# Performance work log

Hardware: AMD Instinct MI355X
Metric: run time of the kernel (lower is better)

## Reference

```python
import jax, jax.numpy as jnp
import numpy as np

B, L1, L2, H = 32, 512, 512, 768


def setup_inputs() -> dict:
    key = jax.random.key(0)
    k1, k2, k3, k4 = jax.random.split(key, 4)
    x = jax.random.normal(k1, (B, L1, H), dtype=jnp.float32)
    y = jax.random.normal(k2, (B, L2, H), dtype=jnp.float32)
    # y_mask: True = padding position to be masked out (torch masked_fill semantics)
    y_mask = jax.random.randint(k3, (B, L2), 0, 2).astype(bool)
    W = jax.random.normal(k4, (H, H), dtype=jnp.float32) * 0.02  # nn.Linear weight [out,in]
    b = jnp.zeros((H,), dtype=jnp.float32)
    return {"x": x, "y": y, "y_mask": y_mask, "W": W, "b": b}


def reference(x, y, y_mask, W, b):
    # Shared linear projection + ReLU on both sequences (nn.Linear: v @ W^T + b)
    x_proj = jax.nn.relu(jnp.einsum('bmh,oh->bmo', x, W) + b)
    y_proj = jax.nn.relu(jnp.einsum('bnh,oh->bno', y, W) + b)
    # Unscaled attention scores [B, L1, L2]
    scores = jnp.einsum('bmh,bnh->bmn', x_proj, y_proj)
    scores = jnp.where(y_mask[:, None, :], -jnp.inf, scores)
    alpha = jax.nn.softmax(scores, axis=-1)
    # Attention-weighted sum over the *original* y (not y_proj)
    matched_seq = jnp.einsum('bmn,bnh->bmh', alpha, y)
    return matched_seq
```

## Files before the change

kernel.cpp:

```cpp
#include <hip/hip_runtime.h>
#include <hip/hip_bf16.h>
#include <math.h>


typedef _Float16 f16x8 __attribute__((ext_vector_type(8)));
typedef float f32x4 __attribute__((ext_vector_type(4)));

__device__ __forceinline__ void gld_lds16(const void* g, void* l) {
  __builtin_amdgcn_global_load_lds(
      (const __attribute__((address_space(1))) unsigned*)g,
      (__attribute__((address_space(3))) unsigned*)l, 16, 0, 0);
}

#define BARR()                          \
  do {                                  \
    __builtin_amdgcn_s_barrier();       \
    __builtin_amdgcn_sched_barrier(0);  \
  } while (0)
#define LGKM0()                                        \
  do {                                                 \
    asm volatile("s_waitcnt lgkmcnt(0)" ::: "memory"); \
    __builtin_amdgcn_sched_barrier(0);                 \
  } while (0)
#define VMW(n)                                            \
  do {                                                    \
    asm volatile("s_waitcnt vmcnt(" #n ")" ::: "memory"); \
    __builtin_amdgcn_sched_barrier(0);                    \
  } while (0)

__global__ __launch_bounds__(256) void cvt_xy_kernel(
    const float* __restrict__ x, const float* __restrict__ y,
    _Float16* __restrict__ xh, _Float16* __restrict__ yh) {
  const float* src = blockIdx.y ? y : x;
  _Float16* dst = blockIdx.y ? yh : xh;
  size_t i = ((size_t)blockIdx.x * 256 + threadIdx.x) * 8;
  float4 a = *(const float4*)&src[i];
  float4 b = *(const float4*)&src[i + 4];
  _Float16 h[8] = {(_Float16)a.x, (_Float16)a.y, (_Float16)a.z, (_Float16)a.w,
                   (_Float16)b.x, (_Float16)b.y, (_Float16)b.z, (_Float16)b.w};
  *(uint4*)&dst[i] = *(uint4*)h;
}

__global__ __launch_bounds__(256) void cvt_f16_kernel(
    const float* __restrict__ src, _Float16* __restrict__ dst) {
  size_t i = ((size_t)blockIdx.x * 256 + threadIdx.x) * 8;
  float4 a = *(const float4*)&src[i];
  float4 b = *(const float4*)&src[i + 4];
  _Float16 h[8] = {(_Float16)a.x, (_Float16)a.y, (_Float16)a.z, (_Float16)a.w,
                   (_Float16)b.x, (_Float16)b.y, (_Float16)b.z, (_Float16)b.w};
  *(uint4*)&dst[i] = *(uint4*)h;
}


__device__ __forceinline__ void stage128(const _Float16* __restrict__ G,
                                         int grow0, int k0, _Float16* L,
                                         int w, int l) {
#pragma unroll
  for (int s = 0; s < 2; ++s) {
    int rb = s * 64 + w * 8;
    int rin = rb + (l >> 3);
    int cp = (l & 7) ^ ((rin >> 1) & 6);
    gld_lds16(&G[(size_t)(grow0 + rin) * 768 + k0 + cp * 8],
              L + (size_t)rb * 64);
  }
}

__device__ __forceinline__ f16x8 frag_ld(const _Float16* S, int row, int colb) {
  int off = row * 128 + colb;
  off ^= (off >> 4) & 0x60;
  return *(const f16x8*)((const char*)S + off);
}

__device__ __forceinline__ void read_a(const _Float16* S, int wm, int mh,
                                       int fr, int fkg, f16x8 a[4][2]) {
#pragma unroll
  for (int f4 = 0; f4 < 4; ++f4)
#pragma unroll
    for (int ks = 0; ks < 2; ++ks)
      a[f4][ks] = frag_ld(S, wm + mh * 64 + f4 * 16 + fr, ks * 64 + fkg * 16);
}

__device__ __forceinline__ void read_b(const _Float16* S, int wn, int nf,
                                       int fr, int fkg, f16x8 b2[2]) {
#pragma unroll
  for (int ks = 0; ks < 2; ++ks)
    b2[ks] = frag_ld(S, wn + nf * 16 + fr, ks * 64 + fkg * 16);
}

__device__ __forceinline__ void mma8(f16x8 a[4][2], f16x8 b2[2],
                                     f32x4 acc[8][2], int mh, int nf) {
#pragma unroll
  for (int ks = 0; ks < 2; ++ks)
#pragma unroll
    for (int f4 = 0; f4 < 4; ++f4)
      acc[mh * 4 + f4][nf] = __builtin_amdgcn_mfma_f32_16x16x32_f16(
          a[f4][ks], b2[ks], acc[mh * 4 + f4][nf], 0, 0, 0);
}

__global__ __launch_bounds__(512, 2) void proj8_kernel(
    const _Float16* __restrict__ Xh, const _Float16* __restrict__ Yh,
    const _Float16* __restrict__ W, const float* __restrict__ bias,
    _Float16* __restrict__ Px, _Float16* __restrict__ Py) {
  const int N = 768;
  const _Float16* A = blockIdx.z ? Yh : Xh;
  _Float16* P = blockIdx.z ? Py : Px;
  extern __shared__ _Float16 smem[];
  _Float16* As0 = smem;
  _Float16* As1 = smem + 16384;
  _Float16* Bs0 = smem + 32768;
  _Float16* Bs1 = smem + 40960;

  const int bm = blockIdx.x * 256, bn = blockIdx.y * 128;
  const int tid = threadIdx.x, l = tid & 63, w = tid >> 6;
  const int fr = l & 15, fkg = l >> 4;
  const int wm = (w >> 2) * 128, wn = (w & 3) * 32;

  f32x4 acc[8][2];
#pragma unroll
  for (int i = 0; i < 8; ++i)
#pragma unroll
    for (int j = 0; j < 2; ++j)
#pragma unroll
      for (int e = 0; e < 4; ++e) acc[i][j][e] = 0.f;

  stage128(A, bm + 0, 0, As0, w, l);
  stage128(A, bm + 128, 0, As0 + 8192, w, l);
  stage128(W, bn, 0, Bs0, w, l);
  stage128(W, bn, 64, Bs1, w, l);
  VMW(2);
  BARR();

  f16x8 a[4][2], b0[2], b1[2];

  for (int t = 0; t < 6; ++t) {
    const bool g = (t < 5);
    const int ko = (2 * t + 1) * 64, ke = (2 * t + 2) * 64, kb = (2 * t + 3) * 64;
    read_a(As0, wm, 0, fr, fkg, a);
    read_b(Bs0, wn, 0, fr, fkg, b0);
    stage128(A, bm + 0, ko, As1, w, l);
    BARR(); LGKM0();
    __builtin_amdgcn_s_setprio(1);
    mma8(a, b0, acc, 0, 0);
    __builtin_amdgcn_s_setprio(0);
    BARR();
    read_b(Bs0, wn, 1, fr, fkg, b1);
    stage128(A, bm + 128, ko, As1 + 8192, w, l);
    BARR(); LGKM0();
    __builtin_amdgcn_s_setprio(1);
    mma8(a, b1, acc, 0, 1);
    __builtin_amdgcn_s_setprio(0);
    BARR();
    read_a(As0, wm, 1, fr, fkg, a);
    if (g) stage128(W, bn, ke, Bs0, w, l);
    BARR(); LGKM0();
    __builtin_amdgcn_s_setprio(1);
    mma8(a, b1, acc, 1, 1);
    mma8(a, b0, acc, 1, 0);
    __builtin_amdgcn_s_setprio(0);
    if (g) { VMW(2); } else { VMW(0); }
    BARR();
    read_a(As1, wm, 0, fr, fkg, a);
    read_b(Bs1, wn, 0, fr, fkg, b0);
    if (g) stage128(A, bm + 0, ke, As0, w, l);
    BARR(); LGKM0();
    __builtin_amdgcn_s_setprio(1);
    mma8(a, b0, acc, 0, 0);
    __builtin_amdgcn_s_setprio(0);
    BARR();
    read_b(Bs1, wn, 1, fr, fkg, b1);
    if (g) stage128(A, bm + 128, ke, As0 + 8192, w, l);
    BARR(); LGKM0();
    __builtin_amdgcn_s_setprio(1);
    mma8(a, b1, acc, 0, 1);
    __builtin_amdgcn_s_setprio(0);
    BARR();
    read_a(As1, wm, 1, fr, fkg, a);
    if (g) stage128(W, bn, kb, Bs1, w, l);
    BARR(); LGKM0();
    __builtin_amdgcn_s_setprio(1);
    mma8(a, b1, acc, 1, 1);
    mma8(a, b0, acc, 1, 0);
    __builtin_amdgcn_s_setprio(0);
    if (g) { VMW(2); } else { VMW(0); }
    BARR();
  }

#pragma unroll
  for (int mf = 0; mf < 8; ++mf)
#pragma unroll
    for (int r = 0; r < 4; ++r) {
      int m = bm + wm + mf * 16 + fkg * 4 + r;
#pragma unroll
      for (int nf = 0; nf < 2; ++nf) {
        int n = bn + wn + nf * 16 + fr;
        P[(size_t)m * N + n] = (_Float16)fmaxf(acc[mf][nf][r] + bias[n], 0.f);
      }
    }
}

__global__ __launch_bounds__(512) void scores_softmax_kernel(
    const _Float16* __restrict__ Px, const _Float16* __restrict__ Py,
    const int* __restrict__ mask, _Float16* __restrict__ Alpha) {
  const int K = 768, L = 512;
  __shared__ _Float16 As[64 * 32];
  __shared__ _Float16 Bs[512 * 32];
  __shared__ float redm[8][64], reds[8][64];
  int b = blockIdx.y;
  size_t pb = (size_t)b * L * K;
  const int* mk = mask + (size_t)b * L;
  _Float16* Ab = Alpha + (size_t)b * L * L;
  int bm = blockIdx.x * 64;
  int tid = threadIdx.x, lane = tid & 63, wave = tid >> 6;
  int wn = wave * 64;
  int fr = lane & 15, fk = (lane >> 4) * 8;
  int lrow = lane >> 2, lcol = (lane & 3) << 3;

  f32x4 acc[4][4];
#pragma unroll
  for (int i = 0; i < 4; ++i)
#pragma unroll
    for (int j = 0; j < 4; ++j)
#pragma unroll
      for (int e = 0; e < 4; ++e) acc[i][j][e] = 0.f;

  for (int k0 = 0; k0 < K; k0 += 32) {
    __syncthreads();
#pragma unroll
    for (int t = 0; t < 4; ++t) {
      int row = wave * 64 + t * 16;
      gld_lds16(&Py[pb + (size_t)(row + lrow) * K + k0 + lcol], &Bs[row * 32]);
    }
    if (wave < 4) {
      int row = wave * 16;
      gld_lds16(&Px[pb + (size_t)(bm + row + lrow) * K + k0 + lcol], &As[row * 32]);
    }
    __syncthreads();
    f16x8 a[4], bb[4];
#pragma unroll
    for (int i = 0; i < 4; ++i) {
      a[i] = *(const f16x8*)&As[(i * 16 + fr) * 32 + fk];
      bb[i] = *(const f16x8*)&Bs[(wn + i * 16 + fr) * 32 + fk];
    }
#pragma unroll
    for (int i = 0; i < 4; ++i)
#pragma unroll
      for (int j = 0; j < 4; ++j)
        acc[i][j] = __builtin_amdgcn_mfma_f32_16x16x32_f16(a[i], bb[j], acc[i][j], 0, 0, 0);
  }

  int mki[4];
#pragma unroll
  for (int j = 0; j < 4; ++j) mki[j] = mk[wn + j * 16 + fr];
#pragma unroll
  for (int i = 0; i < 4; ++i)
#pragma unroll
    for (int j = 0; j < 4; ++j)
      if (mki[j]) {
#pragma unroll
        for (int r = 0; r < 4; ++r) acc[i][j][r] = -INFINITY;
      }

  int g4 = (lane >> 4) << 2;
#pragma unroll
  for (int i = 0; i < 4; ++i)
#pragma unroll
    for (int r = 0; r < 4; ++r) {
      float m = fmaxf(fmaxf(acc[i][0][r], acc[i][1][r]),
                      fmaxf(acc[i][2][r], acc[i][3][r]));
      m = fmaxf(m, __shfl_xor(m, 1));
      m = fmaxf(m, __shfl_xor(m, 2));
      m = fmaxf(m, __shfl_xor(m, 4));
      m = fmaxf(m, __shfl_xor(m, 8));
      if (fr == 0) redm[wave][i * 16 + g4 + r] = m;
    }
  __syncthreads();
  float M[4][4];
#pragma unroll
  for (int i = 0; i < 4; ++i)
#pragma unroll
    for (int r = 0; r < 4; ++r) {
      int row = i * 16 + g4 + r;
      float m = redm[0][row];
#pragma unroll
      for (int ww = 1; ww < 8; ++ww) m = fmaxf(m, redm[ww][row]);
      M[i][r] = m;
    }
#pragma unroll
  for (int i = 0; i < 4; ++i)
#pragma unroll
    for (int r = 0; r < 4; ++r) {
      float s = 0.f;
#pragma unroll
      for (int j = 0; j < 4; ++j) {
        float e = __expf(acc[i][j][r] - M[i][r]);
        acc[i][j][r] = e;
        s += e;
      }
      s += __shfl_xor(s, 1);
      s += __shfl_xor(s, 2);
      s += __shfl_xor(s, 4);
      s += __shfl_xor(s, 8);
      if (fr == 0) reds[wave][i * 16 + g4 + r] = s;
    }
  __syncthreads();
#pragma unroll
  for (int i = 0; i < 4; ++i)
#pragma unroll
    for (int r = 0; r < 4; ++r) {
      int row = i * 16 + g4 + r;
      float s = reds[0][row];
#pragma unroll
      for (int ww = 1; ww < 8; ++ww) s += reds[ww][row];
      float inv = 1.0f / s;
#pragma unroll
      for (int j = 0; j < 4; ++j)
        Ab[(size_t)(bm + row) * L + wn + j * 16 + fr] =
            (_Float16)(acc[i][j][r] * inv);
    }
}

__global__ __launch_bounds__(256) void yT_kernel(
    const _Float16* __restrict__ Yh, _Float16* __restrict__ YT) {
  __shared__ unsigned short T[64][65];
  int b = blockIdx.z;
  int n0 = blockIdx.x * 64, h0 = blockIdx.y * 64;
  const unsigned short* Yb = (const unsigned short*)Yh + (size_t)b * 512 * 768;
  unsigned short* Tb = (unsigned short*)YT + (size_t)b * 768 * 512;
  int tid = threadIdx.x;
  int r = tid >> 4, c = (tid & 15) << 2;
#pragma unroll
  for (int i = 0; i < 4; ++i) {
    int rr = r + i * 16;
    ushort4 v = *(const ushort4*)&Yb[(size_t)(n0 + rr) * 768 + h0 + c];
    T[c + 0][rr] = v.x;
    T[c + 1][rr] = v.y;
    T[c + 2][rr] = v.z;
    T[c + 3][rr] = v.w;
  }
  __syncthreads();
  int hr = tid >> 2, nc = (tid & 3) << 4;
  unsigned short tmp[16];
#pragma unroll
  for (int j = 0; j < 16; ++j) tmp[j] = T[hr][nc + j];
  unsigned short* dst = &Tb[(size_t)(h0 + hr) * 512 + n0 + nc];
  *(uint4*)&dst[0] = *(uint4*)&tmp[0];
  *(uint4*)&dst[8] = *(uint4*)&tmp[8];
}

__global__ __launch_bounds__(256) void attn_mfma_kernel(
    const _Float16* __restrict__ Alpha, const _Float16* __restrict__ YT,
    float* __restrict__ O) {
  const int L = 512, H = 768;
  __shared__ _Float16 As[128 * 32], Bs[128 * 32];
  int b = blockIdx.z;
  const _Float16* Ab = Alpha + (size_t)b * L * L;
  const _Float16* Yb = YT + (size_t)b * H * L;
  float* Ob = O + (size_t)b * L * H;
  int bm = blockIdx.x * 128, bn = blockIdx.y * 128;
  int tid = threadIdx.x, lane = tid & 63, wave = tid >> 6;
  int wm = (wave & 1) * 64, wn = (wave >> 1) * 64;
  int fr = lane & 15, fk = (lane >> 4) * 8;
  int lrow = lane >> 2, lcol = (lane & 3) << 3;

  f32x4 acc[4][4];
#pragma unroll
  for (int i = 0; i < 4; ++i)
#pragma unroll
    for (int j = 0; j < 4; ++j)
#pragma unroll
      for (int e = 0; e < 4; ++e) acc[i][j][e] = 0.f;

  for (int k0 = 0; k0 < L; k0 += 32) {
    __syncthreads();
#pragma unroll
    for (int t = 0; t < 2; ++t) {
      int row = wave * 32 + t * 16;
      gld_lds16(&Ab[(size_t)(bm + row + lrow) * L + k0 + lcol], &As[row * 32]);
      gld_lds16(&Yb[(size_t)(bn + row + lrow) * L + k0 + lcol], &Bs[row * 32]);
    }
    __syncthreads();
    f16x8 a[4], bb[4];
#pragma unroll
    for (int i = 0; i < 4; ++i) {
      a[i] = *(const f16x8*)&As[(wm + i * 16 + fr) * 32 + fk];
      bb[i] = *(const f16x8*)&Bs[(wn + i * 16 + fr) * 32 + fk];
    }
#pragma unroll
    for (int i = 0; i < 4; ++i)
#pragma unroll
      for (int j = 0; j < 4; ++j)
        acc[i][j] = __builtin_amdgcn_mfma_f32_16x16x32_f16(a[i], bb[j], acc[i][j], 0, 0, 0);
  }
#pragma unroll
  for (int i = 0; i < 4; ++i)
#pragma unroll
    for (int r = 0; r < 4; ++r) {
      int m = bm + wm + i * 16 + (lane >> 4) * 4 + r;
#pragma unroll
      for (int j = 0; j < 4; ++j) {
        int h = bn + wn + j * 16 + fr;
        Ob[(size_t)m * H + h] = acc[i][j][r];
      }
    }
}

extern "C" void kernel_launch(void* const* d_in, const int* in_sizes, int n_in,
                              void* d_out, int out_size, void* d_ws, size_t ws_size,
                              hipStream_t stream) {
  const float* x = (const float*)d_in[0];
  const float* y = (const float*)d_in[1];
  const int* y_mask = (const int*)d_in[2];
  const float* W = (const float*)d_in[3];
  const float* b = (const float*)d_in[4];
  float* out = (float*)d_out;

  const size_t E = (size_t)16384 * 768;
  _Float16* xh = (_Float16*)d_ws;
  _Float16* yh = xh + E;
  _Float16* Px = yh + E;
  _Float16* Py = Px + E;
  _Float16* Wh = Py + E;
  _Float16* alpha = xh;
  _Float16* yT = Px;

  static bool attr_set = false;
  if (!attr_set) {
    hipFuncSetAttribute((const void*)proj8_kernel,
                        hipFuncAttributeMaxDynamicSharedMemorySize, 98304);
    attr_set = true;
  }

  dim3 blk(256);
  cvt_xy_kernel<<<dim3(6144, 2), blk, 0, stream>>>(x, y, xh, yh);
  cvt_f16_kernel<<<dim3(288), blk, 0, stream>>>(W, Wh);
  proj8_kernel<<<dim3(64, 6, 2), dim3(512), 98304, stream>>>(xh, yh, Wh, b, Px, Py);
  scores_softmax_kernel<<<dim3(8, 32), dim3(512), 0, stream>>>(Px, Py, y_mask, alpha);
  yT_kernel<<<dim3(8, 12, 32), blk, 0, stream>>>(yh, yT);
  attn_mfma_kernel<<<dim3(4, 6, 32), blk, 0, stream>>>(alpha, yT, out);
}
```

Before: 288.0 us.

## Fuse y conversion with transpose, remap grids for XCD locality, retune LDS swizzle

Converts y to fp16 and writes its transpose in one kernel, removing the separate transpose pass that reread fp16 y. Merges the x and W conversions into one launch. Changes the LDS XOR swizzle to use the low three row bits, aiming to reduce bank conflicts. Linearizes the scores and attention grids so neighbouring blocks scheduled on different XCDs map to distinct batches, improving L2 locality. yT now needs a separate workspace region.

```diff
diff --git a/kernel.cpp b/kernel.cpp
--- a/kernel.cpp
+++ b/kernel.cpp
@@ -28,12 +28,20 @@
     __builtin_amdgcn_sched_barrier(0);                    \
   } while (0)
 
-__global__ __launch_bounds__(256) void cvt_xy_kernel(
-    const float* __restrict__ x, const float* __restrict__ y,
-    _Float16* __restrict__ xh, _Float16* __restrict__ yh) {
-  const float* src = blockIdx.y ? y : x;
-  _Float16* dst = blockIdx.y ? yh : xh;
-  size_t i = ((size_t)blockIdx.x * 256 + threadIdx.x) * 8;
+__global__ __launch_bounds__(256) void cvt_xW_kernel(
+    const float* __restrict__ x, const float* __restrict__ W,
+    _Float16* __restrict__ xh, _Float16* __restrict__ Wh) {
+  int bid = blockIdx.x;
+  const float* src;
+  _Float16* dst;
+  size_t i;
+  if (bid < 6144) {
+    src = x; dst = xh;
+    i = ((size_t)bid * 256 + threadIdx.x) * 8;
+  } else {
+    src = W; dst = Wh;
+    i = ((size_t)(bid - 6144) * 256 + threadIdx.x) * 8;
+  }
   float4 a = *(const float4*)&src[i];
   float4 b = *(const float4*)&src[i + 4];
   _Float16 h[8] = {(_Float16)a.x, (_Float16)a.y, (_Float16)a.z, (_Float16)a.w,
@@ -41,14 +49,37 @@
   *(uint4*)&dst[i] = *(uint4*)h;
 }
 
-__global__ __launch_bounds__(256) void cvt_f16_kernel(
-    const float* __restrict__ src, _Float16* __restrict__ dst) {
-  size_t i = ((size_t)blockIdx.x * 256 + threadIdx.x) * 8;
-  float4 a = *(const float4*)&src[i];
-  float4 b = *(const float4*)&src[i + 4];
-  _Float16 h[8] = {(_Float16)a.x, (_Float16)a.y, (_Float16)a.z, (_Float16)a.w,
-                   (_Float16)b.x, (_Float16)b.y, (_Float16)b.z, (_Float16)b.w};
-  *(uint4*)&dst[i] = *(uint4*)h;
+__global__ __launch_bounds__(256) void cvt_y_yT_kernel(
+    const float* __restrict__ Y, _Float16* __restrict__ Yh,
+    _Float16* __restrict__ YT) {
+  __shared__ unsigned short T[64][65];
+  int b = blockIdx.z;
+  int n0 = blockIdx.x * 64, h0 = blockIdx.y * 64;
+  const float* Yb = Y + (size_t)b * 512 * 768;
+  unsigned short* Hb = (unsigned short*)Yh + (size_t)b * 512 * 768;
+  unsigned short* Tb = (unsigned short*)YT + (size_t)b * 768 * 512;
+  int tid = threadIdx.x;
+  int r = tid >> 4, c = (tid & 15) << 2;
+#pragma unroll
+  for (int i = 0; i < 4; ++i) {
+    int rr = r + i * 16;
+    float4 v = *(const float4*)&Yb[(size_t)(n0 + rr) * 768 + h0 + c];
+    _Float16 h[4] = {(_Float16)v.x, (_Float16)v.y, (_Float16)v.z, (_Float16)v.w};
+    unsigned short* hu = (unsigned short*)h;
+    T[c + 0][rr] = hu[0];
+    T[c + 1][rr] = hu[1];
+    T[c + 2][rr] = hu[2];
+    T[c + 3][rr] = hu[3];
+    *(ushort4*)&Hb[(size_t)(n0 + rr) * 768 + h0 + c] = *(ushort4*)hu;
+  }
+  __syncthreads();
+  int hr = tid >> 2, nc = (tid & 3) << 4;
+  unsigned short tmp[16];
+#pragma unroll
+  for (int j = 0; j < 16; ++j) tmp[j] = T[hr][nc + j];
+  unsigned short* dst = &Tb[(size_t)(h0 + hr) * 512 + n0 + nc];
+  *(uint4*)&dst[0] = *(uint4*)&tmp[0];
+  *(uint4*)&dst[8] = *(uint4*)&tmp[8];
 }
 
 
@@ -59,7 +90,7 @@
   for (int s = 0; s < 2; ++s) {
     int rb = s * 64 + w * 8;
     int rin = rb + (l >> 3);
-    int cp = (l & 7) ^ ((rin >> 1) & 6);
+    int cp = (l & 7) ^ (rin & 7);
     gld_lds16(&G[(size_t)(grow0 + rin) * 768 + k0 + cp * 8],
               L + (size_t)rb * 64);
   }
@@ -67,7 +98,7 @@
 
 __device__ __forceinline__ f16x8 frag_ld(const _Float16* S, int row, int colb) {
   int off = row * 128 + colb;
-  off ^= (off >> 4) & 0x60;
+  off ^= (row & 7) << 4;
   return *(const f16x8*)((const char*)S + off);
 }
 
@@ -205,11 +236,13 @@
   __shared__ _Float16 As[64 * 32];
   __shared__ _Float16 Bs[512 * 32];
   __shared__ float redm[8][64], reds[8][64];
-  int b = blockIdx.y;
+  int g = blockIdx.x;
+  int xr = g & 7, k = g >> 3;
+  int b = (k >> 3) * 8 + xr;
+  int bm = (k & 7) * 64;
   size_t pb = (size_t)b * L * K;
   const int* mk = mask + (size_t)b * L;
   _Float16* Ab = Alpha + (size_t)b * L * L;
-  int bm = blockIdx.x * 64;
   int tid = threadIdx.x, lane = tid & 63, wave = tid >> 6;
   int wn = wave * 64;
   int fr = lane & 15, fk = (lane >> 4) * 8;
@@ -319,44 +352,19 @@
     }
 }
 
-__global__ __launch_bounds__(256) void yT_kernel(
-    const _Float16* __restrict__ Yh, _Float16* __restrict__ YT) {
-  __shared__ unsigned short T[64][65];
-  int b = blockIdx.z;
-  int n0 = blockIdx.x * 64, h0 = blockIdx.y * 64;
-  const unsigned short* Yb = (const unsigned short*)Yh + (size_t)b * 512 * 768;
-  unsigned short* Tb = (unsigned short*)YT + (size_t)b * 768 * 512;
-  int tid = threadIdx.x;
-  int r = tid >> 4, c = (tid & 15) << 2;
-#pragma unroll
-  for (int i = 0; i < 4; ++i) {
-    int rr = r + i * 16;
-    ushort4 v = *(const ushort4*)&Yb[(size_t)(n0 + rr) * 768 + h0 + c];
-    T[c + 0][rr] = v.x;
-    T[c + 1][rr] = v.y;
-    T[c + 2][rr] = v.z;
-    T[c + 3][rr] = v.w;
-  }
-  __syncthreads();
-  int hr = tid >> 2, nc = (tid & 3) << 4;
-  unsigned short tmp[16];
-#pragma unroll
-  for (int j = 0; j < 16; ++j) tmp[j] = T[hr][nc + j];
-  unsigned short* dst = &Tb[(size_t)(h0 + hr) * 512 + n0 + nc];
-  *(uint4*)&dst[0] = *(uint4*)&tmp[0];
-  *(uint4*)&dst[8] = *(uint4*)&tmp[8];
-}
-
 __global__ __launch_bounds__(256) void attn_mfma_kernel(
     const _Float16* __restrict__ Alpha, const _Float16* __restrict__ YT,
     float* __restrict__ O) {
   const int L = 512, H = 768;
   __shared__ _Float16 As[128 * 32], Bs[128 * 32];
-  int b = blockIdx.z;
+  int g = blockIdx.x;
+  int xr = g & 7, k = g >> 3;
+  int b = (k / 24) * 8 + xr;
+  int j24 = k % 24;
+  int bm = (j24 & 3) * 128, bn = (j24 >> 2) * 128;
   const _Float16* Ab = Alpha + (size_t)b * L * L;
   const _Float16* Yb = YT + (size_t)b * H * L;
   float* Ob = O + (size_t)b * L * H;
-  int bm = blockIdx.x * 128, bn = blockIdx.y * 128;
   int tid = threadIdx.x, lane = tid & 63, wave = tid >> 6;
   int wm = (wave & 1) * 64, wn = (wave >> 1) * 64;
   int fr = lane & 15, fk = (lane >> 4) * 8;
@@ -420,8 +428,8 @@
   _Float16* Px = yh + E;
   _Float16* Py = Px + E;
   _Float16* Wh = Py + E;
+  _Float16* yT = Wh + (size_t)768 * 768;
   _Float16* alpha = xh;
-  _Float16* yT = Px;
 
   static bool attr_set = false;
   if (!attr_set) {
@@ -431,10 +439,9 @@
   }
 
   dim3 blk(256);
-  cvt_xy_kernel<<<dim3(6144, 2), blk, 0, stream>>>(x, y, xh, yh);
-  cvt_f16_kernel<<<dim3(288), blk, 0, stream>>>(W, Wh);
+  cvt_xW_kernel<<<dim3(6144 + 288), blk, 0, stream>>>(x, W, xh, Wh);
+  cvt_y_yT_kernel<<<dim3(8, 12, 32), blk, 0, stream>>>(y, yh, yT);
   proj8_kernel<<<dim3(64, 6, 2), dim3(512), 98304, stream>>>(xh, yh, Wh, b, Px, Py);
-  scores_softmax_kernel<<<dim3(8, 32), dim3(512), 0, stream>>>(Px, Py, y_mask, alpha);
-  yT_kernel<<<dim3(8, 12, 32), blk, 0, stream>>>(yh, yT);
-  attn_mfma_kernel<<<dim3(4, 6, 32), blk, 0, stream>>>(alpha, yT, out);
-}
+  scores_softmax_kernel<<<dim3(256), dim3(512), 0, stream>>>(Px, Py, y_mask, alpha);
+  attn_mfma_kernel<<<dim3(768), blk, 0, stream>>>(alpha, yT, out);
+}
```

Result: faster. 270.6 us (-6.0%).
